# Performance work log

Measured on AMD Instinct MI355X. Metric: run time of the kernel, lower is better.

Reference implementation:

```python
import jax, jax.numpy as jnp
import numpy as np

B, S, D, H = 512, 128, 2, 512


def _lstm_cell(x, h, c, Wih, Whh, bih, bhh):
    # PyTorch gate order: i, f, g, o
    z = x @ Wih.T + h @ Whh.T + bih + bhh
    i, f, g, o = jnp.split(z, 4, axis=-1)
    c = jax.nn.sigmoid(f) * c + jax.nn.sigmoid(i) * jnp.tanh(g)
    h = jax.nn.sigmoid(o) * jnp.tanh(c)
    return h, c


def setup_inputs() -> dict:
    key = jax.random.key(0)
    ks = jax.random.split(key, 18)
    sc = 1.0 / np.sqrt(H)
    u = lambda k, shape: jax.random.uniform(k, shape, jnp.float32, -sc, sc)
    return {
        "inp": jax.random.normal(ks[0], (B, S, D), jnp.float32),
        "enc_Wih": u(ks[1], (4 * H, D)),
        "enc_Whh": u(ks[2], (4 * H, H)),
        "enc_bih": u(ks[3], (4 * H,)),
        "enc_bhh": u(ks[4], (4 * H,)),
        "dec_Wih": u(ks[5], (4 * H, D)),
        "dec_Whh": u(ks[6], (4 * H, H)),
        "dec_bih": u(ks[7], (4 * H,)),
        "dec_bhh": u(ks[8], (4 * H,)),
        "W1": u(ks[9], (H, H)),
        "b1": u(ks[10], (H,)),
        "W2": u(ks[11], (H, H)),
        "b2": u(ks[12], (H,)),
        "v_w": u(ks[13], (H,)),
        "v_b": u(ks[14], (1,)),
        "comb_W": u(ks[15], (H, 2 * H)),
        "comb_b": u(ks[16], (H,)),
    }


def reference(inp, enc_Wih, enc_Whh, enc_bih, enc_bhh,
              dec_Wih, dec_Whh, dec_bih, dec_bhh,
              W1, b1, W2, b2, v_w, v_b, comb_W, comb_b):
    Bb, Ss, _ = inp.shape
    xs = jnp.transpose(inp, (1, 0, 2))  # [S,B,D]

    # --- encoder LSTM (1 layer) ---
    def enc_step(carry, x):
        h, c = carry
        h, c = _lstm_cell(x, h, c, enc_Wih, enc_Whh, enc_bih, enc_bhh)
        return (h, c), h

    h0 = jnp.zeros((Bb, H), inp.dtype)
    (h_enc, c_enc), enc_out = jax.lax.scan(enc_step, (h0, h0), xs)  # enc_out: [S,B,H]

    W1e = enc_out @ W1.T + b1            # [S,B,H]
    enc_bt = jnp.transpose(enc_out, (1, 0, 2))  # [B,S,H]

    # --- pointer decoder ---
    def dec_step(carry, _):
        h, c, cur = carry
        h, c = _lstm_cell(cur, h, c, dec_Wih, dec_Whh, dec_bih, dec_bhh)
        q = h @ W2.T + b2                               # [B,H]
        u = jnp.tanh(W1e + q[None]) @ v_w + v_b[0]      # [S,B]
        a = jax.nn.softmax(u.T, axis=1)                 # [B,S]
        chosen = jnp.argmax(a, axis=1)                  # [B]
        cur = jnp.take_along_axis(inp, chosen[:, None, None], axis=1)[:, 0, :]  # [B,D]
        ctx = jnp.einsum('bs,bsh->bh', a, enc_bt)       # [B,H]
        h = jnp.concatenate([ctx, h], axis=1) @ comb_W.T + comb_b
        return (h, c, cur), a

    cur0 = jnp.full((Bb, D), -1.0, inp.dtype)
    _, outs = jax.lax.scan(dec_step, (h_enc, c_enc, cur0), None, length=Ss)
    return jnp.transpose(outs, (1, 0, 2))  # [B,S,S]
```

## Files before the change

### kernel.cpp

```cpp
#include <hip/hip_runtime.h>

#define PB 512
#define PS 128
#define PD 2
#define PH 512
#define P4H 2048

typedef unsigned int u32;
typedef unsigned short u16;
typedef __attribute__((ext_vector_type(8))) short short8;
typedef __attribute__((ext_vector_type(4))) float f32x4;

__device__ __forceinline__ float fast_sigmoid(float x) {
    return __fdividef(1.0f, 1.0f + __expf(-x));
}
__device__ __forceinline__ float fast_tanh(float x) {
    float ax = fabsf(x);
    float e = __expf(-2.0f * ax);
    float r = __fdividef(1.0f - e, 1.0f + e);
    return x < 0.0f ? -r : r;
}

__device__ __forceinline__ float bf_dec_u(u16 v) { return __uint_as_float((u32)v << 16); }
__device__ __forceinline__ u16 bf_trunc(float v) { return (u16)(__float_as_uint(v) >> 16); }
__device__ __forceinline__ u16 bf_rne(float v) {
    u32 u = __float_as_uint(v);
    return (u16)((u + 0x7FFFu + ((u >> 16) & 1u)) >> 16);
}
__device__ __forceinline__ void bf_split(float v, u16& hi, u16& lo) {
    hi = bf_trunc(v);
    lo = bf_rne(v - bf_dec_u(hi));
}

struct CF32 {
    using T = float;
    static __device__ __forceinline__ float dec(T v) { return v; }
    static __device__ __forceinline__ T enc(float v) { return v; }
    static __device__ __forceinline__ void dec4(const T* p, float* o) {
        float4 v = *(const float4*)p; o[0]=v.x; o[1]=v.y; o[2]=v.z; o[3]=v.w;
    }
};
struct CBF16 {
    using T = u16;
    static __device__ __forceinline__ float dec(T v) { return __uint_as_float((u32)v << 16); }
    static __device__ __forceinline__ T enc(float v) { return bf_rne(v); }
    static __device__ __forceinline__ void dec4(const T* p, float* o) {
        uint2 v = *(const uint2*)p;
        o[0] = __uint_as_float(v.x << 16);
        o[1] = __uint_as_float(v.x & 0xFFFF0000u);
        o[2] = __uint_as_float(v.y << 16);
        o[3] = __uint_as_float(v.y & 0xFFFF0000u);
    }
};

__global__ __launch_bounds__(256) void prep_whh(
    const float* __restrict__ Whh, u16* __restrict__ hi, u16* __restrict__ lo,
    float* __restrict__ f32out)
{
    int np = blockIdx.x;
    int j = np >> 2, g = np & 3;
    const float* src = Whh + (size_t)(g * PH + j) * PH;
    for (int k = threadIdx.x; k < PH; k += 256) {
        float v = src[k];
        u16 h_, l_;
        bf_split(v, h_, l_);
        hi[(size_t)np * PH + k] = h_;
        lo[(size_t)np * PH + k] = l_;
        if (f32out) f32out[(size_t)np * PH + k] = v;
    }
}
__global__ __launch_bounds__(256) void prep_split(
    const float* __restrict__ W, u16* __restrict__ hi, u16* __restrict__ lo, int K)
{
    int n = blockIdx.x;
    const float* src = W + (size_t)n * K;
    for (int k = threadIdx.x; k < K; k += 256) {
        u16 h_, l_;
        bf_split(src[k], h_, l_);
        hi[(size_t)n * K + k] = h_;
        lo[(size_t)n * K + k] = l_;
    }
}
__global__ __launch_bounds__(256) void prep_transpose_split(
    const float* __restrict__ W, u16* __restrict__ hi, u16* __restrict__ lo)
{
    __shared__ float tile[32][33];
    int m0 = blockIdx.x * 32;
    int k0 = blockIdx.y * 32;
    int tx = threadIdx.x & 31, ty = threadIdx.x >> 5;
    #pragma unroll
    for (int i = 0; i < 4; ++i) {
        int k = k0 + ty + i * 8;
        tile[ty + i * 8][tx] = W[(size_t)k * (2 * PH) + m0 + tx];
    }
    __syncthreads();
    #pragma unroll
    for (int i = 0; i < 4; ++i) {
        int m = m0 + ty + i * 8;
        float v = tile[tx][ty + i * 8];
        u16 h_, l_; bf_split(v, h_, l_);
        hi[(size_t)m * PH + k0 + tx] = h_;
        lo[(size_t)m * PH + k0 + tx] = l_;
    }
}
__global__ __launch_bounds__(256) void prep_small(
    const float* __restrict__ Wih, const float* __restrict__ bih,
    const float* __restrict__ bhh, float* __restrict__ wihp, float* __restrict__ bs)
{
    int np = blockIdx.x * 256 + threadIdx.x;
    if (np >= P4H) return;
    int j = np >> 2, g = np & 3;
    int n = g * PH + j;
    wihp[np * 2]     = Wih[(size_t)n * PD];
    wihp[np * 2 + 1] = Wih[(size_t)n * PD + 1];
    bs[np] = bih[n] + bhh[n];
}
__global__ __launch_bounds__(256) void prep_bfused(
    const float* __restrict__ whh_f32p, const float* __restrict__ comb_b,
    const float* __restrict__ bsum_d, float* __restrict__ bf)
{
    int np = blockIdx.x * 4 + (threadIdx.x >> 6);
    int lane = threadIdx.x & 63;
    const float* wr = whh_f32p + (size_t)np * PH + lane * 8;
    const float* cb = comb_b + lane * 8;
    float s = 0.0f;
    #pragma unroll
    for (int i = 0; i < 8; ++i) s += wr[i] * cb[i];
    #pragma unroll
    for (int off = 32; off; off >>= 1) s += __shfl_xor(s, off);
    if (lane == 0) bf[np] = s + bsum_d[np];
}

template<int EXTRA_MODE, int KK>
__global__ __launch_bounds__(256) void lstm_fused(
    const u16* __restrict__ Whh_hi, const u16* __restrict__ Whh_lo,
    const float* __restrict__ wih_perm, const float* __restrict__ bsum,
    const float* __restrict__ x, int x_stride,
    const float* __restrict__ h_in,
    float* __restrict__ cT,
    float* __restrict__ h_out,
    void* __restrict__ extra, int ex_stride)
{
    __shared__ u16 As_hi[64][72];
    __shared__ u16 As_lo[64][72];
    __shared__ u16 Bs_hi[64][72];
    __shared__ u16 Bs_lo[64][72];

    const int tid = threadIdx.x;
    const int bb = blockIdx.x * 64;
    const int bn = blockIdx.y * 64;
    const int w = tid >> 6;
    const int wm = w >> 1, wn = w & 1;
    const int lane = tid & 63;
    const int l15 = lane & 15, lq = lane >> 4;

    f32x4 acc[2][2];
    #pragma unroll
    for (int i = 0; i < 2; ++i)
        #pragma unroll
        for (int j = 0; j < 2; ++j)
            acc[i][j] = (f32x4)0.0f;

    for (int k0 = 0; k0 < KK; k0 += 64) {
        #pragma unroll
        for (int rep = 0; rep < 2; ++rep) {
            int chunk = tid + rep * 256;
            int row = chunk >> 3, kc = (chunk & 7) * 8;
            *(uint4*)&As_hi[row][kc] = *(const uint4*)&Whh_hi[(size_t)(bn + row) * KK + k0 + kc];
            *(uint4*)&As_lo[row][kc] = *(const uint4*)&Whh_lo[(size_t)(bn + row) * KK + k0 + kc];
        }
        #pragma unroll
        for (int rep = 0; rep < 4; ++rep) {
            int chunk = tid + rep * 256;
            int row = chunk >> 4, kc = (chunk & 15) * 4;
            float4 v = *(const float4*)&h_in[(size_t)(bb + row) * KK + k0 + kc];
            u16 h0_, l0_, h1_, l1_, h2_, l2_, h3_, l3_;
            bf_split(v.x, h0_, l0_); bf_split(v.y, h1_, l1_);
            bf_split(v.z, h2_, l2_); bf_split(v.w, h3_, l3_);
            *(uint2*)&Bs_hi[row][kc] = make_uint2((u32)h0_ | ((u32)h1_ << 16),
                                                  (u32)h2_ | ((u32)h3_ << 16));
            *(uint2*)&Bs_lo[row][kc] = make_uint2((u32)l0_ | ((u32)l1_ << 16),
                                                  (u32)l2_ | ((u32)l3_ << 16));
        }
        __syncthreads();
        #pragma unroll
        for (int ks = 0; ks < 2; ++ks) {
            int kk = ks * 32 + lq * 8;
            short8 ah[2], al[2], bh[2], bl[2];
            #pragma unroll
            for (int mf = 0; mf < 2; ++mf) {
                int r = wm * 32 + mf * 16 + l15;
                ah[mf] = *(const short8*)&As_hi[r][kk];
                al[mf] = *(const short8*)&As_lo[r][kk];
            }
            #pragma unroll
            for (int nf = 0; nf < 2; ++nf) {
                int r = wn * 32 + nf * 16 + l15;
                bh[nf] = *(const short8*)&Bs_hi[r][kk];
                bl[nf] = *(const short8*)&Bs_lo[r][kk];
            }
            #pragma unroll
            for (int mf = 0; mf < 2; ++mf)
                #pragma unroll
                for (int nf = 0; nf < 2; ++nf) {
                    acc[mf][nf] = __builtin_amdgcn_mfma_f32_16x16x32_bf16(ah[mf], bh[nf], acc[mf][nf], 0, 0, 0);
                    acc[mf][nf] = __builtin_amdgcn_mfma_f32_16x16x32_bf16(ah[mf], bl[nf], acc[mf][nf], 0, 0, 0);
                    acc[mf][nf] = __builtin_amdgcn_mfma_f32_16x16x32_bf16(al[mf], bh[nf], acc[mf][nf], 0, 0, 0);
                }
        }
        __syncthreads();
    }

    float* Hs = (float*)&As_hi[0][0];
    #pragma unroll
    for (int nf = 0; nf < 2; ++nf) {
        int b_loc = wn * 32 + nf * 16 + l15;
        int b = bb + b_loc;
        float x0 = x[b * x_stride];
        float x1 = x[b * x_stride + 1];
        #pragma unroll
        for (int mf = 0; mf < 2; ++mf) {
            int np_loc = wm * 32 + mf * 16 + lq * 4;
            int np = bn + np_loc;
            float4 b4 = *(const float4*)&bsum[np];
            float4 wA = *(const float4*)&wih_perm[np * 2];
            float4 wB = *(const float4*)&wih_perm[np * 2 + 4];
            float zi = acc[mf][nf][0] + b4.x + x0 * wA.x + x1 * wA.y;
            float zf = acc[mf][nf][1] + b4.y + x0 * wA.z + x1 * wA.w;
            float zg = acc[mf][nf][2] + b4.z + x0 * wB.x + x1 * wB.y;
            float zo = acc[mf][nf][3] + b4.w + x0 * wB.z + x1 * wB.w;
            int jg = np >> 2;
            float cold = cT[(size_t)jg * PB + b];
            float cv = fast_sigmoid(zf) * cold + fast_sigmoid(zi) * fast_tanh(zg);
            float hv = fast_sigmoid(zo) * fast_tanh(cv);
            cT[(size_t)jg * PB + b] = cv;
            Hs[(np_loc >> 2) * 66 + b_loc] = hv;
        }
    }
    __syncthreads();
    {
        int b_loc = tid >> 2, jp = (tid & 3) * 4;
        int b = bb + b_loc;
        int jbase = bn >> 2;
        float4 hv4;
        hv4.x = Hs[(jp + 0) * 66 + b_loc];
        hv4.y = Hs[(jp + 1) * 66 + b_loc];
        hv4.z = Hs[(jp + 2) * 66 + b_loc];
        hv4.w = Hs[(jp + 3) * 66 + b_loc];
        *(float4*)&h_out[(size_t)b * PH + jbase + jp] = hv4;
        if (EXTRA_MODE == 1) {
            u16* e = (u16*)extra;
            *(uint2*)&e[(size_t)b * ex_stride + jbase + jp] =
                make_uint2((u32)bf_rne(hv4.x) | ((u32)bf_rne(hv4.y) << 16),
                           (u32)bf_rne(hv4.z) | ((u32)bf_rne(hv4.w) << 16));
        } else if (EXTRA_MODE == 2) {
            float* e = (float*)extra;
            *(float4*)&e[(size_t)b * ex_stride + jbase + jp] = hv4;
        }
    }
}

template<int ACT_F32, int OUTMODE>
__global__ __launch_bounds__(256) void gemm_wtA(
    const u16* __restrict__ Whi, const u16* __restrict__ Wlo,
    const void* __restrict__ act, const float* __restrict__ bias,
    void* __restrict__ out, void* __restrict__ out2, int K, int ldo)
{
    __shared__ u16 As_hi[64][72];
    __shared__ u16 As_lo[64][72];
    __shared__ u16 Bs_hi[64][72];
    __shared__ u16 Bs_lo[64][72];

    const int tid = threadIdx.x;
    const int bm = blockIdx.x * 64;
    const int bn = blockIdx.y * 64;
    const int w = tid >> 6;
    const int wm = w >> 1, wn = w & 1;
    const int lane = tid & 63;
    const int l15 = lane & 15, lq = lane >> 4;

    f32x4 acc[2][2];
    #pragma unroll
    for (int i = 0; i < 2; ++i)
        #pragma unroll
        for (int j = 0; j < 2; ++j)
            acc[i][j] = (f32x4)0.0f;

    for (int k0 = 0; k0 < K; k0 += 64) {
        #pragma unroll
        for (int rep = 0; rep < 2; ++rep) {
            int chunk = tid + rep * 256;
            int row = chunk >> 3, kc = (chunk & 7) * 8;
            *(uint4*)&As_hi[row][kc] = *(const uint4*)&Whi[(size_t)(bn + row) * K + k0 + kc];
            *(uint4*)&As_lo[row][kc] = *(const uint4*)&Wlo[(size_t)(bn + row) * K + k0 + kc];
        }
        if (ACT_F32) {
            const float* a = (const float*)act;
            #pragma unroll
            for (int rep = 0; rep < 4; ++rep) {
                int chunk = tid + rep * 256;
                int row = chunk >> 4, kc = (chunk & 15) * 4;
                float4 v = *(const float4*)&a[(size_t)(bm + row) * K + k0 + kc];
                u16 h0_, l0_, h1_, l1_, h2_, l2_, h3_, l3_;
                bf_split(v.x, h0_, l0_); bf_split(v.y, h1_, l1_);
                bf_split(v.z, h2_, l2_); bf_split(v.w, h3_, l3_);
                *(uint2*)&Bs_hi[row][kc] = make_uint2((u32)h0_ | ((u32)h1_ << 16),
                                                      (u32)h2_ | ((u32)h3_ << 16));
                *(uint2*)&Bs_lo[row][kc] = make_uint2((u32)l0_ | ((u32)l1_ << 16),
                                                      (u32)l2_ | ((u32)l3_ << 16));
            }
        } else {
            const u16* a = (const u16*)act;
            #pragma unroll
            for (int rep = 0; rep < 2; ++rep) {
                int chunk = tid + rep * 256;
                int row = chunk >> 3, kc = (chunk & 7) * 8;
                *(uint4*)&Bs_hi[row][kc] = *(const uint4*)&a[(size_t)(bm + row) * K + k0 + kc];
            }
        }
        __syncthreads();
        #pragma unroll
        for (int ks = 0; ks < 2; ++ks) {
            int kk = ks * 32 + lq * 8;
            short8 ah[2], al[2], bh[2], bl[2];
            #pragma unroll
            for (int mf = 0; mf < 2; ++mf) {
                int r = wm * 32 + mf * 16 + l15;
                ah[mf] = *(const short8*)&As_hi[r][kk];
                al[mf] = *(const short8*)&As_lo[r][kk];
            }
            #pragma unroll
            for (int nf = 0; nf < 2; ++nf) {
                int r = wn * 32 + nf * 16 + l15;
                bh[nf] = *(const short8*)&Bs_hi[r][kk];
                if (ACT_F32) bl[nf] = *(const short8*)&Bs_lo[r][kk];
            }
            #pragma unroll
            for (int mf = 0; mf < 2; ++mf)
                #pragma unroll
                for (int nf = 0; nf < 2; ++nf) {
                    acc[mf][nf] = __builtin_amdgcn_mfma_f32_16x16x32_bf16(ah[mf], bh[nf], acc[mf][nf], 0, 0, 0);
                    if (ACT_F32) {
                        acc[mf][nf] = __builtin_amdgcn_mfma_f32_16x16x32_bf16(ah[mf], bl[nf], acc[mf][nf], 0, 0, 0);
                        acc[mf][nf] = __builtin_amdgcn_mfma_f32_16x16x32_bf16(al[mf], bh[nf], acc[mf][nf], 0, 0, 0);
                    } else {
                        acc[mf][nf] = __builtin_amdgcn_mfma_f32_16x16x32_bf16(al[mf], bh[nf], acc[mf][nf], 0, 0, 0);
                    }
                }
        }
        __syncthreads();
    }

    #pragma unroll
    for (int nf = 0; nf < 2; ++nf) {
        int m = bm + wn * 32 + nf * 16 + l15;
        #pragma unroll
        for (int mf = 0; mf < 2; ++mf) {
            int n = bn + wm * 32 + mf * 16 + lq * 4;
            float4 b4 = bias ? *(const float4*)&bias[n] : make_float4(0.f, 0.f, 0.f, 0.f);
            float v0 = acc[mf][nf][0] + b4.x;
            float v1 = acc[mf][nf][1] + b4.y;
            float v2 = acc[mf][nf][2] + b4.z;
            float v3 = acc[mf][nf][3] + b4.w;
            if (OUTMODE == 1) {
                u16* o = (u16*)out;
                *(uint2*)&o[(size_t)m * ldo + n] =
                    make_uint2((u32)bf_rne(v0) | ((u32)bf_rne(v1) << 16),
                               (u32)bf_rne(v2) | ((u32)bf_rne(v3) << 16));
            } else if (OUTMODE == 2) {
                u16 h0_, l0_, h1_, l1_, h2_, l2_, h3_, l3_;
                bf_split(v0, h0_, l0_); bf_split(v1, h1_, l1_);
                bf_split(v2, h2_, l2_); bf_split(v3, h3_, l3_);
                u16* oh = (u16*)out;
                u16* ol = (u16*)out2;
                *(uint2*)&oh[(size_t)m * ldo + n] =
                    make_uint2((u32)h0_ | ((u32)h1_ << 16), (u32)h2_ | ((u32)h3_ << 16));
                *(uint2*)&ol[(size_t)m * ldo + n] =
                    make_uint2((u32)l0_ | ((u32)l1_ << 16), (u32)l2_ | ((u32)l3_ << 16));
            } else {
                float* o = (float*)out;
                *(float4*)&o[(size_t)m * ldo + n] = make_float4(v0, v1, v2, v3);
            }
        }
    }
}

__global__ __launch_bounds__(256) void attn_fused(
    const u16* __restrict__ W1e,
    const u16* __restrict__ enc_out,
    const float* __restrict__ qv,
    const float* __restrict__ v_w, const float* __restrict__ v_b,
    const float* __restrict__ inp,
    float* __restrict__ out,
    float* __restrict__ cat_out,
    float* __restrict__ cur, int t)
{
    __shared__ float u_s[PS];
    __shared__ float a_s[PS];
    const int b = blockIdx.x;
    const int tid = threadIdx.x;
    const int w = tid >> 6, lane = tid & 63;

    float q8[8], v8[8];
    {
        const float* qr = qv + (size_t)b * PH + lane * 8;
        CF32::dec4(qr, q8); CF32::dec4(qr + 4, q8 + 4);
        const float* vr = v_w + lane * 8;
        CF32::dec4(vr, v8); CF32::dec4(vr + 4, v8 + 4);
    }
    const float vb = v_b[0];
    const u16* wbase = W1e + (size_t)b * PS * PH + lane * 8;
    #pragma unroll 2
    for (int i = 0; i < 32; ++i) {
        int s = w * 32 + i;
        const u16* row = wbase + (size_t)s * PH;
        float w8[8];
        CBF16::dec4(row, w8); CBF16::dec4(row + 4, w8 + 4);
        float sum = 0.0f;
        #pragma unroll
        for (int j = 0; j < 8; ++j) sum += v8[j] * fast_tanh(w8[j] + q8[j]);
        #pragma unroll
        for (int off = 32; off; off >>= 1) sum += __shfl_xor(sum, off);
        if (lane == 0) u_s[s] = sum + vb;
    }
    __syncthreads();
    if (w == 0) {
        float2 uv = make_float2(u_s[lane * 2], u_s[lane * 2 + 1]);
        float m = fmaxf(uv.x, uv.y);
        int mi = (uv.y > uv.x) ? (lane * 2 + 1) : (lane * 2);
        #pragma unroll
        for (int off = 32; off; off >>= 1) {
            float om = __shfl_xor(m, off);
            int oi = __shfl_xor(mi, off);
            if (om > m || (om == m && oi < mi)) { m = om; mi = oi; }
        }
        float e0 = __expf(uv.x - m);
        float e1 = __expf(uv.y - m);
        float ssum = e0 + e1;
        #pragma unroll
        for (int off = 32; off; off >>= 1) ssum += __shfl_xor(ssum, off);
        float inv = __fdividef(1.0f, ssum);
        float2 av = make_float2(e0 * inv, e1 * inv);
        a_s[lane * 2] = av.x; a_s[lane * 2 + 1] = av.y;
        *(float2*)&out[(size_t)b * PS * PS + (size_t)t * PS + lane * 2] = av;
        if (lane == 0) {
            cur[b * 2]     = inp[(size_t)b * PS * PD + mi * PD];
            cur[b * 2 + 1] = inp[(size_t)b * PS * PD + mi * PD + 1];
        }
    }
    __syncthreads();
    float acc0 = 0.0f, acc1 = 0.0f;
    const u16* ebase = enc_out + (size_t)b * PS * PH + tid * 2;
    #pragma unroll 4
    for (int s = 0; s < PS; ++s) {
        float a = a_s[s];
        u32 pr = *(const u32*)(ebase + (size_t)s * PH);
        acc0 = fmaf(a, __uint_as_float(pr << 16), acc0);
        acc1 = fmaf(a, __uint_as_float(pr & 0xFFFF0000u), acc1);
    }
    *(float2*)&cat_out[(size_t)b * (2 * PH) + tid * 2] = make_float2(acc0, acc1);
}

template<class C>
__global__ __launch_bounds__(256) void u_pass(
    const typename C::T* __restrict__ W1e, const float* __restrict__ q,
    const float* __restrict__ v_w, const float* __restrict__ v_b,
    float* __restrict__ u_t)
{
    int row = blockIdx.x * 4 + (threadIdx.x >> 6);
    int lane = threadIdx.x & 63;
    int s = row >> 9;
    int b = row & (PB - 1);
    const typename C::T* wr = W1e + (size_t)row * PH + lane * 8;
    const float* qr = q + (size_t)b * PH + lane * 8;
    const float* vr = v_w + lane * 8;
    float w8[8], q8[8], v8[8];
    C::dec4(wr, w8); C::dec4(wr + 4, w8 + 4);
    CF32::dec4(qr, q8); CF32::dec4(qr + 4, q8 + 4);
    CF32::dec4(vr, v8); CF32::dec4(vr + 4, v8 + 4);
    float sum = 0.0f;
    #pragma unroll
    for (int i = 0; i < 8; ++i)
        sum += v8[i] * fast_tanh(w8[i] + q8[i]);
    #pragma unroll
    for (int off = 32; off; off >>= 1) sum += __shfl_xor(sum, off);
    if (lane == 0) u_t[b * PS + s] = sum + v_b[0];
}

__global__ __launch_bounds__(256) void softmax_step(
    const float* __restrict__ u_t, const float* __restrict__ inp,
    float* __restrict__ a_buf, float* __restrict__ out,
    float* __restrict__ cur, int t)
{
    int b = blockIdx.x * 4 + (threadIdx.x >> 6);
    int lane = threadIdx.x & 63;
    float2 uv = *(const float2*)&u_t[b * PS + lane * 2];
    float m = fmaxf(uv.x, uv.y);
    int mi = (uv.y > uv.x) ? (lane * 2 + 1) : (lane * 2);
    #pragma unroll
    for (int off = 32; off; off >>= 1) {
        float om = __shfl_xor(m, off);
        int oi = __shfl_xor(mi, off);
        if (om > m || (om == m && oi < mi)) { m = om; mi = oi; }
    }
    float e0 = __expf(uv.x - m);
    float e1 = __expf(uv.y - m);
    float ssum = e0 + e1;
    #pragma unroll
    for (int off = 32; off; off >>= 1) ssum += __shfl_xor(ssum, off);
    float inv = __fdividef(1.0f, ssum);
    float2 av = make_float2(e0 * inv, e1 * inv);
    *(float2*)&a_buf[b * PS + lane * 2] = av;
    *(float2*)&out[(size_t)b * PS * PS + (size_t)t * PS + lane * 2] = av;
    if (lane == 0) {
        cur[b * 2]     = inp[(size_t)b * PS * PD + mi * PD];
        cur[b * 2 + 1] = inp[(size_t)b * PS * PD + mi * PD + 1];
    }
}

template<class C>
__global__ __launch_bounds__(256) void ctx_kernel(
    const typename C::T* __restrict__ enc_out, const float* __restrict__ a_buf,
    float* __restrict__ catbuf)
{
    int b = blockIdx.x;
    int hidx = threadIdx.x;
    const float* ab = a_buf + b * PS;
    const typename C::T* e = enc_out + (size_t)b * PH;
    float acc0 = 0.0f, acc1 = 0.0f;
    #pragma unroll 4
    for (int s = 0; s < PS; ++s) {
        float a = ab[s];
        const typename C::T* es = e + (size_t)s * PB * PH;
        acc0 = fmaf(a, C::dec(es[hidx]), acc0);
        acc1 = fmaf(a, C::dec(es[hidx + 256]), acc1);
    }
    catbuf[(size_t)b * (2 * PH) + hidx] = acc0;
    catbuf[(size_t)b * (2 * PH) + hidx + 256] = acc1;
}

__global__ __launch_bounds__(256) void init_kernel(
    float* __restrict__ h, float* __restrict__ c, float* __restrict__ cur)
{
    int i = blockIdx.x * 256 + threadIdx.x;
    if (i < PB * PH) { h[i] = 0.0f; c[i] = 0.0f; }
    if (i < PB * PD) cur[i] = -1.0f;
}

template<class CA, class CO, int BM, int BN, int BK, int TM, int TN>
__global__ __launch_bounds__(256) void gemm_nt(
    const typename CA::T* __restrict__ A, const float* __restrict__ Bm,
    const float* __restrict__ bias, typename CO::T* __restrict__ C,
    int M, int N, int K)
{
    __shared__ float As[BK][BM];
    __shared__ float Bs[BK][BN];
    constexpr int TCOLS = BN / TN;
    constexpr int TROWS = BM / TM;
    static_assert(TCOLS * TROWS == 256, "thread tiling");
    const int tid = threadIdx.x;
    const int tc = tid % TCOLS;
    const int tr = tid / TCOLS;
    const int bm = blockIdx.y * BM;
    const int bn = blockIdx.x * BN;
    constexpr int AF4 = BM * BK / 4;
    constexpr int BF4 = BN * BK / 4;
    constexpr int KQ  = BK / 4;
    float acc[TM][TN];
    #pragma unroll
    for (int m = 0; m < TM; ++m)
        #pragma unroll
        for (int n = 0; n < TN; ++n) acc[m][n] = 0.0f;
    for (int k0 = 0; k0 < K; k0 += BK) {
        #pragma unroll
        for (int i = tid; i < AF4; i += 256) {
            int r = i / KQ, kq = i % KQ;
            float v4[4];
            CA::dec4(A + (size_t)(bm + r) * K + k0 + kq * 4, v4);
            As[kq*4+0][r] = v4[0]; As[kq*4+1][r] = v4[1];
            As[kq*4+2][r] = v4[2]; As[kq*4+3][r] = v4[3];
        }
        #pragma unroll
        for (int i = tid; i < BF4; i += 256) {
            int r = i / KQ, kq = i % KQ;
            const float4 v = *(const float4*)(Bm + (size_t)(bn + r) * K + k0 + kq * 4);
            Bs[kq*4+0][r] = v.x; Bs[kq*4+1][r] = v.y;
            Bs[kq*4+2][r] = v.z; Bs[kq*4+3][r] = v.w;
        }
        __syncthreads();
        #pragma unroll
        for (int k = 0; k < BK; ++k) {
            float av[TM], bv[TN];
            #pragma unroll
            for (int m = 0; m < TM; ++m) av[m] = As[k][tr * TM + m];
            #pragma unroll
            for (int n = 0; n < TN; ++n) bv[n] = Bs[k][tc * TN + n];
            #pragma unroll
            for (int m = 0; m < TM; ++m)
                #pragma unroll
                for (int n = 0; n < TN; ++n)
                    acc[m][n] = fmaf(av[m], bv[n], acc[m][n]);
        }
        __syncthreads();
    }
    #pragma unroll
    for (int m = 0; m < TM; ++m) {
        int row = bm + tr * TM + m;
        #pragma unroll
        for (int n = 0; n < TN; ++n) {
            int col = bn + tc * TN + n;
            float v = acc[m][n];
            if (bias) v += bias[col];
            C[(size_t)row * N + col] = CO::enc(v);
        }
    }
}

template<class CE>
__global__ __launch_bounds__(256) void lstm_cell(
    const float* __restrict__ z,
    const float* __restrict__ x, int x_stride,
    const float* __restrict__ Wih,
    const float* __restrict__ bih, const float* __restrict__ bhh,
    float* __restrict__ c, float* __restrict__ h,
    typename CE::T* __restrict__ extra, int extra_stride)
{
    int idx = blockIdx.x * 256 + threadIdx.x;
    int b = idx >> 9, j = idx & (PH - 1);
    float x0 = x[b * x_stride];
    float x1 = x[b * x_stride + 1];
    const float* zr = z + (size_t)b * P4H;
    float zi = zr[j]        + bih[j]        + bhh[j]        + x0 * Wih[2*j]          + x1 * Wih[2*j+1];
    float zf = zr[j + PH]   + bih[j + PH]   + bhh[j + PH]   + x0 * Wih[2*(j+PH)]     + x1 * Wih[2*(j+PH)+1];
    float zg = zr[j + 2*PH] + bih[j + 2*PH] + bhh[j + 2*PH] + x0 * Wih[2*(j+2*PH)]   + x1 * Wih[2*(j+2*PH)+1];
    float zo = zr[j + 3*PH] + bih[j + 3*PH] + bhh[j + 3*PH] + x0 * Wih[2*(j+3*PH)]   + x1 * Wih[2*(j+3*PH)+1];
    float cv = fast_sigmoid(zf) * c[idx] + fast_sigmoid(zi) * fast_tanh(zg);
    float hv = fast_sigmoid(zo) * fast_tanh(cv);
    c[idx] = cv;
    h[idx] = hv;
    if (extra) extra[(size_t)b * extra_stride + j] = CE::enc(hv);
}

struct Inputs {
    const float *inp, *enc_Wih, *enc_Whh, *enc_bih, *enc_bhh;
    const float *dec_Wih, *dec_Whh, *dec_bih, *dec_bhh;
    const float *W1, *b1, *W2, *b2, *v_w, *v_b, *comb_W, *comb_b;
};
static Inputs unpack(void* const* d_in) {
    Inputs in;
    in.inp = (const float*)d_in[0];
    in.enc_Wih = (const float*)d_in[1]; in.enc_Whh = (const float*)d_in[2];
    in.enc_bih = (const float*)d_in[3]; in.enc_bhh = (const float*)d_in[4];
    in.dec_Wih = (const float*)d_in[5]; in.dec_Whh = (const float*)d_in[6];
    in.dec_bih = (const float*)d_in[7]; in.dec_bhh = (const float*)d_in[8];
    in.W1 = (const float*)d_in[9];  in.b1 = (const float*)d_in[10];
    in.W2 = (const float*)d_in[11]; in.b2 = (const float*)d_in[12];
    in.v_w = (const float*)d_in[13]; in.v_b = (const float*)d_in[14];
    in.comb_W = (const float*)d_in[15]; in.comb_b = (const float*)d_in[16];
    return in;
}

static const size_t BIG = (size_t)PS * PB * PH;

static void run_mfma2(const Inputs& in, float* out, void* d_ws, hipStream_t stream)
{
    char* p = (char*)d_ws;
    auto alloc = [&](size_t bytes) { char* r = p; p += bytes; return r; };
    u16* enc_out  = (u16*)alloc(BIG * 2);
    u16* W1e      = (u16*)alloc(BIG * 2);
    u16* whh_e_hi = (u16*)alloc((size_t)P4H * PH * 2);
    u16* whh_e_lo = (u16*)alloc((size_t)P4H * PH * 2);
    u16* whh_d_hi = (u16*)alloc((size_t)P4H * PH * 2);
    u16* whh_d_lo = (u16*)alloc((size_t)P4H * PH * 2);
    u16* w1h = (u16*)alloc((size_t)PH * PH * 2);
    u16* w1l = (u16*)alloc((size_t)PH * PH * 2);
    u16* w2h = (u16*)alloc((size_t)PH * PH * 2);
    u16* w2l = (u16*)alloc((size_t)PH * PH * 2);
    u16* ctw_h = (u16*)alloc((size_t)(2 * PH) * PH * 2);
    u16* ctw_l = (u16*)alloc((size_t)(2 * PH) * PH * 2);
    u16* wf_h = (u16*)alloc((size_t)P4H * (2 * PH) * 2);
    u16* wf_l = (u16*)alloc((size_t)P4H * (2 * PH) * 2);
    float* wih_e = (float*)alloc((size_t)P4H * 2 * 4);
    float* wih_d = (float*)alloc((size_t)P4H * 2 * 4);
    float* bsum_e = (float*)alloc((size_t)P4H * 4);
    float* bsum_d = (float*)alloc((size_t)P4H * 4);
    float* b_fus  = (float*)alloc((size_t)P4H * 4);
    float* hpp0 = (float*)alloc((size_t)PB * PH * 4);
    float* hpp1 = (float*)alloc((size_t)PB * PH * 4);
    float* cT   = (float*)alloc((size_t)PB * PH * 4);
    float* catreg = (float*)alloc((size_t)PB * 2 * PH * 4 * 2);
    float* cur  = (float*)alloc((size_t)PB * PD * 4);
    float* whh_f32p = catreg;
    float* h0 = (float*)whh_e_hi;
    float* q  = (float*)whh_e_lo;
    float* cat[2] = { catreg, catreg + (size_t)PB * 2 * PH };
    float* hpp[2] = { hpp0, hpp1 };

    prep_whh<<<P4H, 256, 0, stream>>>(in.enc_Whh, whh_e_hi, whh_e_lo, nullptr);
    prep_whh<<<P4H, 256, 0, stream>>>(in.dec_Whh, whh_d_hi, whh_d_lo, whh_f32p);
    prep_split<<<PH, 256, 0, stream>>>(in.W1, w1h, w1l, PH);
    prep_split<<<PH, 256, 0, stream>>>(in.W2, w2h, w2l, PH);
    prep_transpose_split<<<dim3(32, 16), 256, 0, stream>>>(in.comb_W, ctw_h, ctw_l);
    prep_small<<<P4H / 256, 256, 0, stream>>>(in.enc_Wih, in.enc_bih, in.enc_bhh, wih_e, bsum_e);
    prep_small<<<P4H / 256, 256, 0, stream>>>(in.dec_Wih, in.dec_bih, in.dec_bhh, wih_d, bsum_d);
    gemm_wtA<1, 2><<<dim3(P4H / 64, (2 * PH) / 64), 256, 0, stream>>>(
        ctw_h, ctw_l, whh_f32p, nullptr, wf_h, wf_l, PH, 2 * PH);
    prep_bfused<<<P4H / 4, 256, 0, stream>>>(whh_f32p, in.comb_b, bsum_d, b_fus);
    init_kernel<<<1024, 256, 0, stream>>>(hpp0, cT, cur);

    for (int s = 0; s < PS; ++s) {
        lstm_fused<1, PH><<<dim3(PB / 64, P4H / 64), 256, 0, stream>>>(
            whh_e_hi, whh_e_lo, wih_e, bsum_e,
            in.inp + s * PD, PS * PD,
            hpp[s & 1], cT, hpp[(s + 1) & 1],
            enc_out + (size_t)s * PH, PS * PH);
    }

    gemm_wtA<0, 1><<<dim3((PS * PB) / 64, PH / 64), 256, 0, stream>>>(
        w1h, w1l, enc_out, in.b1, W1e, nullptr, PH, PH);

    for (int t = 0; t < PS; ++t) {
        float* cat_out = cat[(t + 1) & 1];
        if (t == 0) {
            lstm_fused<2, PH><<<dim3(PB / 64, P4H / 64), 256, 0, stream>>>(
                whh_d_hi, whh_d_lo, wih_d, bsum_d,
                cur, PD, hpp[0], cT, h0, cat_out + PH, 2 * PH);
        } else {
            lstm_fused<2, 2 * PH><<<dim3(PB / 64, P4H / 64), 256, 0, stream>>>(
                wf_h, wf_l, wih_d, b_fus,
                cur, PD, cat[t & 1], cT, h0, cat_out + PH, 2 * PH);
        }
        gemm_wtA<1, 0><<<dim3(PB / 64, PH / 64), 256, 0, stream>>>(
            w2h, w2l, h0, in.b2, q, nullptr, PH, PH);
        attn_fused<<<PB, 256, 0, stream>>>(
            W1e, enc_out, q, in.v_w, in.v_b, in.inp, out, cat_out, cur, t);
    }
}

static void run_mfma(const Inputs& in, float* out, void* d_ws, hipStream_t stream)
{
    char* p = (char*)d_ws;
    auto alloc = [&](size_t bytes) { char* r = p; p += bytes; return r; };
    u16* enc_out = (u16*)alloc(BIG * 2);
    u16* W1e     = (u16*)alloc(BIG * 2);
    u16* whh_e_hi = (u16*)alloc((size_t)P4H * PH * 2);
    u16* whh_e_lo = (u16*)alloc((size_t)P4H * PH * 2);
    u16* whh_d_hi = (u16*)alloc((size_t)P4H * PH * 2);
    u16* whh_d_lo = (u16*)alloc((size_t)P4H * PH * 2);
    u16* w1h = (u16*)alloc((size_t)PH * PH * 2);
    u16* w1l = (u16*)alloc((size_t)PH * PH * 2);
    u16* w2h = (u16*)alloc((size_t)PH * PH * 2);
    u16* w2l = (u16*)alloc((size_t)PH * PH * 2);
    u16* cwh = (u16*)alloc((size_t)PH * 2 * PH * 2);
    u16* cwl = (u16*)alloc((size_t)PH * 2 * PH * 2);
    float* wih_e = (float*)alloc((size_t)P4H * 2 * 4);
    float* wih_d = (float*)alloc((size_t)P4H * 2 * 4);
    float* bsum_e = (float*)alloc((size_t)P4H * 4);
    float* bsum_d = (float*)alloc((size_t)P4H * 4);
    float* hpp0 = (float*)alloc((size_t)PB * PH * 4);
    float* hpp1 = (float*)alloc((size_t)PB * PH * 4);
    float* cT   = (float*)alloc((size_t)PB * PH * 4);
    float* h0   = (float*)alloc((size_t)PB * PH * 4);
    float* q    = (float*)alloc((size_t)PB * PH * 4);
    float* catbuf = (float*)alloc((size_t)PB * 2 * PH * 4);
    float* u_t  = (float*)alloc((size_t)PB * PS * 4);
    float* a_buf = (float*)alloc((size_t)PB * PS * 4);
    float* cur  = (float*)alloc((size_t)PB * PD * 4);
    float* hpp[2] = { hpp0, hpp1 };

    prep_whh<<<P4H, 256, 0, stream>>>(in.enc_Whh, whh_e_hi, whh_e_lo, nullptr);
    prep_whh<<<P4H, 256, 0, stream>>>(in.dec_Whh, whh_d_hi, whh_d_lo, nullptr);
    prep_split<<<PH, 256, 0, stream>>>(in.W1, w1h, w1l, PH);
    prep_split<<<PH, 256, 0, stream>>>(in.W2, w2h, w2l, PH);
    prep_split<<<PH, 256, 0, stream>>>(in.comb_W, cwh, cwl, 2 * PH);
    prep_small<<<P4H / 256, 256, 0, stream>>>(in.enc_Wih, in.enc_bih, in.enc_bhh, wih_e, bsum_e);
    prep_small<<<P4H / 256, 256, 0, stream>>>(in.dec_Wih, in.dec_bih, in.dec_bhh, wih_d, bsum_d);
    init_kernel<<<1024, 256, 0, stream>>>(hpp0, cT, cur);

    for (int s = 0; s < PS; ++s) {
        lstm_fused<1, PH><<<dim3(PB / 64, P4H / 64), 256, 0, stream>>>(
            whh_e_hi, whh_e_lo, wih_e, bsum_e,
            in.inp + s * PD, PS * PD,
            hpp[s & 1], cT, hpp[(s + 1) & 1],
            enc_out + (size_t)s * PB * PH, PH);
    }
    gemm_wtA<0, 1><<<dim3((PS * PB) / 64, PH / 64), 256, 0, stream>>>(
        w1h, w1l, enc_out, in.b1, W1e, nullptr, PH, PH);
    for (int t = 0; t < PS; ++t) {
        lstm_fused<2, PH><<<dim3(PB / 64, P4H / 64), 256, 0, stream>>>(
            whh_d_hi, whh_d_lo, wih_d, bsum_d,
            cur, PD, hpp[t & 1], cT, h0, catbuf + PH, 2 * PH);
        gemm_wtA<1, 0><<<dim3(PB / 64, PH / 64), 256, 0, stream>>>(
            w2h, w2l, h0, in.b2, q, nullptr, PH, PH);
        u_pass<CBF16><<<(PS * PB) / 4, 256, 0, stream>>>(W1e, q, in.v_w, in.v_b, u_t);
        softmax_step<<<PB / 4, 256, 0, stream>>>(u_t, in.inp, a_buf, out, cur, t);
        ctx_kernel<CBF16><<<PB, 256, 0, stream>>>(enc_out, a_buf, catbuf);
        gemm_wtA<1, 0><<<dim3(PB / 64, PH / 64), 256, 0, stream>>>(
            cwh, cwl, catbuf, in.comb_b, hpp[(t + 1) & 1], nullptr, 2 * PH, PH);
    }
}

static void run_fallback(const Inputs& in, float* out, void* d_ws, hipStream_t stream)
{
    char* p = (char*)d_ws;
    u16* enc_out = (u16*)p;  p += BIG * 2;
    u16* W1e     = (u16*)p;  p += BIG * 2;
    float* ws = (float*)p;
    size_t off = 0;
    auto alloc = [&](size_t n) { float* r = ws + off; off += n; return r; };
    float* z      = alloc((size_t)PB * P4H);
    float* h      = alloc((size_t)PB * PH);
    float* c      = alloc((size_t)PB * PH);
    float* h0     = alloc((size_t)PB * PH);
    float* q      = alloc((size_t)PB * PH);
    float* catbuf = alloc((size_t)PB * 2 * PH);
    float* u_t    = alloc((size_t)PB * PS);
    float* a_buf  = alloc((size_t)PB * PS);
    float* cur    = alloc((size_t)PB * PD);

    init_kernel<<<1024, 256, 0, stream>>>(h, c, cur);
    for (int s = 0; s < PS; ++s) {
        gemm_nt<CF32, CF32, 64, 64, 32, 4, 4><<<dim3(P4H / 64, PB / 64), 256, 0, stream>>>(
            h, in.enc_Whh, nullptr, z, PB, P4H, PH);
        lstm_cell<CBF16><<<1024, 256, 0, stream>>>(
            z, in.inp + s * PD, PS * PD, in.enc_Wih, in.enc_bih, in.enc_bhh,
            c, h, enc_out + (size_t)s * PB * PH, PH);
    }
    gemm_nt<CBF16, CBF16, 64, 64, 32, 4, 4><<<dim3(PH / 64, (PS * PB) / 64), 256, 0, stream>>>(
        enc_out, in.W1, in.b1, W1e, PS * PB, PH, PH);
    for (int t = 0; t < PS; ++t) {
        gemm_nt<CF32, CF32, 64, 64, 32, 4, 4><<<dim3(P4H / 64, PB / 64), 256, 0, stream>>>(
            h, in.dec_Whh, nullptr, z, PB, P4H, PH);
        lstm_cell<CF32><<<1024, 256, 0, stream>>>(
            z, cur, PD, in.dec_Wih, in.dec_bih, in.dec_bhh,
            c, h0, catbuf + PH, 2 * PH);
        gemm_nt<CF32, CF32, 32, 32, 32, 2, 2><<<dim3(PH / 32, PB / 32), 256, 0, stream>>>(
            h0, in.W2, in.b2, q, PB, PH, PH);
        u_pass<CBF16><<<(PS * PB) / 4, 256, 0, stream>>>(W1e, q, in.v_w, in.v_b, u_t);
        softmax_step<<<PB / 4, 256, 0, stream>>>(u_t, in.inp, a_buf, out, cur, t);
        ctx_kernel<CBF16><<<PB, 256, 0, stream>>>(enc_out, a_buf, catbuf);
        gemm_nt<CF32, CF32, 32, 32, 32, 2, 2><<<dim3(PH / 32, PB / 32), 256, 0, stream>>>(
            catbuf, in.comb_W, in.comb_b, h, PB, PH, 2 * PH);
    }
}

extern "C" void kernel_launch(void* const* d_in, const int* in_sizes, int n_in,
                              void* d_out, int out_size, void* d_ws, size_t ws_size,
                              hipStream_t stream)
{
    Inputs in = unpack(d_in);
    float* out = (float*)d_out;

    const size_t t1_need =
        BIG * 2 * 2 +
        (size_t)P4H * PH * 2 * 4 +
        (size_t)PH * PH * 2 * 4 +
        (size_t)(2 * PH) * PH * 2 * 2 +
        (size_t)P4H * (2 * PH) * 2 * 2 +
        (size_t)P4H * 2 * 4 * 2 +
        (size_t)P4H * 4 * 3 +
        (size_t)PB * PH * 4 * 3 +
        (size_t)PB * 2 * PH * 4 * 2 +
        (size_t)PB * PD * 4;
    const size_t t2_need =
        BIG * 2 * 2 +
        (size_t)P4H * PH * 2 * 4 +
        (size_t)PH * PH * 2 * 4 +
        (size_t)PH * 2 * PH * 2 * 2 +
        (size_t)P4H * 2 * 4 * 2 +
        (size_t)P4H * 4 * 2 +
        ((size_t)PB * PH * 6 + (size_t)PB * PS * 2 + PB * PD) * 4;
    const size_t t3_need =
        BIG * 2 * 2 +
        ((size_t)PB * P4H + 4 * (size_t)PB * PH + (size_t)PB * 2 * PH +
         2 * (size_t)PB * PS + (size_t)PB * PD) * 4;

    if (ws_size >= t1_need)       run_mfma2(in, out, d_ws, stream);
    else if (ws_size >= t2_need)  run_mfma(in, out, d_ws, stream);
    else if (ws_size >= t3_need)  run_fallback(in, out, d_ws, stream);
}
```

Baseline: 11.78 ms.

## Use 32-row LSTM and q GEMM tiles to raise block count

Adds lstm_fused32, which tiles 32 gate rows by 64 batch rows, and gemm32_f32, which uses 32x32 tiles. Both replace the 64x64 kernels in the encoder and decoder loops, doubling or quadrupling the number of blocks per launch so more CUs are busy on these small per-step GEMMs. Workspace is reorganized: the encoder Whh split, the transposed comb_W and one h ping-pong buffer are aliased into the W1e region, which is only written after the encoder finishes. The cost is smaller tiles with less operand reuse per block, and the aliasing depends on W1e not being produced before the encoder loop ends.

```diff
diff --git a/kernel.cpp b/kernel.cpp
--- a/kernel.cpp
+++ b/kernel.cpp
@@ -129,6 +129,180 @@
     #pragma unroll
     for (int off = 32; off; off >>= 1) s += __shfl_xor(s, off);
     if (lane == 0) bf[np] = s + bsum_d[np];
+}
+
+template<int EXTRA_MODE, int KK>
+__global__ __launch_bounds__(256, 2) void lstm_fused32(
+    const u16* __restrict__ Whh_hi, const u16* __restrict__ Whh_lo,
+    const float* __restrict__ wih_perm, const float* __restrict__ bsum,
+    const float* __restrict__ x, int x_stride,
+    const float* __restrict__ h_in,
+    float* __restrict__ cT,
+    float* __restrict__ h_out,
+    void* __restrict__ extra, int ex_stride)
+{
+    __shared__ u16 As_hi[32][72];
+    __shared__ u16 As_lo[32][72];
+    __shared__ u16 Bs_hi[64][72];
+    __shared__ u16 Bs_lo[64][72];
+
+    const int tid = threadIdx.x;
+    const int bnp = blockIdx.x * 32;
+    const int bb  = blockIdx.y * 64;
+    const int w = tid >> 6;
+    const int wm = w >> 1, wn = w & 1;
+    const int lane = tid & 63;
+    const int l15 = lane & 15, lq = lane >> 4;
+
+    f32x4 acc0 = (f32x4)0.0f, acc1 = (f32x4)0.0f;
+
+    for (int k0 = 0; k0 < KK; k0 += 64) {
+        {
+            int row = tid >> 3, kc = (tid & 7) * 8;
+            *(uint4*)&As_hi[row][kc] = *(const uint4*)&Whh_hi[(size_t)(bnp + row) * KK + k0 + kc];
+            *(uint4*)&As_lo[row][kc] = *(const uint4*)&Whh_lo[(size_t)(bnp + row) * KK + k0 + kc];
+        }
+        #pragma unroll
+        for (int rep = 0; rep < 4; ++rep) {
+            int chunk = tid + rep * 256;
+            int row = chunk >> 4, kc = (chunk & 15) * 4;
+            float4 v = *(const float4*)&h_in[(size_t)(bb + row) * KK + k0 + kc];
+            u16 h0_, l0_, h1_, l1_, h2_, l2_, h3_, l3_;
+            bf_split(v.x, h0_, l0_); bf_split(v.y, h1_, l1_);
+            bf_split(v.z, h2_, l2_); bf_split(v.w, h3_, l3_);
+            *(uint2*)&Bs_hi[row][kc] = make_uint2((u32)h0_ | ((u32)h1_ << 16),
+                                                  (u32)h2_ | ((u32)h3_ << 16));
+            *(uint2*)&Bs_lo[row][kc] = make_uint2((u32)l0_ | ((u32)l1_ << 16),
+                                                  (u32)l2_ | ((u32)l3_ << 16));
+        }
+        __syncthreads();
+        #pragma unroll
+        for (int ks = 0; ks < 2; ++ks) {
+            int kk = ks * 32 + lq * 8;
+            short8 ah, al, bh0, bl0, bh1, bl1;
+            {
+                int r = wm * 16 + l15;
+                ah = *(const short8*)&As_hi[r][kk];
+                al = *(const short8*)&As_lo[r][kk];
+            }
+            {
+                int r = wn * 32 + l15;
+                bh0 = *(const short8*)&Bs_hi[r][kk];
+                bl0 = *(const short8*)&Bs_lo[r][kk];
+                bh1 = *(const short8*)&Bs_hi[r + 16][kk];
+                bl1 = *(const short8*)&Bs_lo[r + 16][kk];
+            }
+            acc0 = __builtin_amdgcn_mfma_f32_16x16x32_bf16(ah, bh0, acc0, 0, 0, 0);
+            acc0 = __builtin_amdgcn_mfma_f32_16x16x32_bf16(ah, bl0, acc0, 0, 0, 0);
+            acc0 = __builtin_amdgcn_mfma_f32_16x16x32_bf16(al, bh0, acc0, 0, 0, 0);
+            acc1 = __builtin_amdgcn_mfma_f32_16x16x32_bf16(ah, bh1, acc1, 0, 0, 0);
+            acc1 = __builtin_amdgcn_mfma_f32_16x16x32_bf16(ah, bl1, acc1, 0, 0, 0);
+            acc1 = __builtin_amdgcn_mfma_f32_16x16x32_bf16(al, bh1, acc1, 0, 0, 0);
+        }
+        __syncthreads();
+    }
+
+    float* Hs = (float*)&As_hi[0][0];
+    const int np_loc = wm * 16 + lq * 4;
+    const int np = bnp + np_loc;
+    const float4 b4 = *(const float4*)&bsum[np];
+    const float4 wA = *(const float4*)&wih_perm[np * 2];
+    const float4 wB = *(const float4*)&wih_perm[np * 2 + 4];
+    const int jg = np >> 2;
+    #pragma unroll
+    for (int nf = 0; nf < 2; ++nf) {
+        int b_loc = wn * 32 + nf * 16 + l15;
+        int b = bb + b_loc;
+        float x0 = x[b * x_stride];
+        float x1 = x[b * x_stride + 1];
+        f32x4 a = nf ? acc1 : acc0;
+        float zi = a[0] + b4.x + x0 * wA.x + x1 * wA.y;
+        float zf = a[1] + b4.y + x0 * wA.z + x1 * wA.w;
+        float zg = a[2] + b4.z + x0 * wB.x + x1 * wB.y;
+        float zo = a[3] + b4.w + x0 * wB.z + x1 * wB.w;
+        float cold = cT[(size_t)jg * PB + b];
+        float cv = fast_sigmoid(zf) * cold + fast_sigmoid(zi) * fast_tanh(zg);
+        float hv = fast_sigmoid(zo) * fast_tanh(cv);
+        cT[(size_t)jg * PB + b] = cv;
+        Hs[(np_loc >> 2) * 66 + b_loc] = hv;
+    }
+    __syncthreads();
+    {
+        int b_loc = tid & 63, jp = (tid >> 6) * 2;
+        int b = bb + b_loc;
+        int jbase = bnp >> 2;
+        float h0v = Hs[jp * 66 + b_loc];
+        float h1v = Hs[(jp + 1) * 66 + b_loc];
+        *(float2*)&h_out[(size_t)b * PH + jbase + jp] = make_float2(h0v, h1v);
+        if (EXTRA_MODE == 1) {
+            u16* e = (u16*)extra;
+            *(u32*)&e[(size_t)b * ex_stride + jbase + jp] =
+                (u32)bf_rne(h0v) | ((u32)bf_rne(h1v) << 16);
+        } else if (EXTRA_MODE == 2) {
+            float* e = (float*)extra;
+            *(float2*)&e[(size_t)b * ex_stride + jbase + jp] = make_float2(h0v, h1v);
+        }
+    }
+}
+
+__global__ __launch_bounds__(256, 2) void gemm32_f32(
+    const u16* __restrict__ Whi, const u16* __restrict__ Wlo,
+    const float* __restrict__ act, const float* __restrict__ bias,
+    float* __restrict__ out, int K, int ldo)
+{
+    __shared__ u16 As_hi[32][72];
+    __shared__ u16 As_lo[32][72];
+    __shared__ u16 Bs_hi[32][72];
+    __shared__ u16 Bs_lo[32][72];
+
+    const int tid = threadIdx.x;
+    const int bn = blockIdx.x * 32;
+    const int bm = blockIdx.y * 32;
+    const int w = tid >> 6;
+    const int wm = w >> 1, wn = w & 1;
+    const int lane = tid & 63, l15 = lane & 15, lq = lane >> 4;
+
+    f32x4 acc = (f32x4)0.0f;
+
+    for (int k0 = 0; k0 < K; k0 += 64) {
+        {
+            int row = tid >> 3, kc = (tid & 7) * 8;
+            *(uint4*)&As_hi[row][kc] = *(const uint4*)&Whi[(size_t)(bn + row) * K + k0 + kc];
+            *(uint4*)&As_lo[row][kc] = *(const uint4*)&Wlo[(size_t)(bn + row) * K + k0 + kc];
+        }
+        #pragma unroll
+        for (int rep = 0; rep < 2; ++rep) {
+            int chunk = tid + rep * 256;
+            int row = chunk >> 4, kc = (chunk & 15) * 4;
+            float4 v = *(const float4*)&act[(size_t)(bm + row) * K + k0 + kc];
+            u16 h0_, l0_, h1_, l1_, h2_, l2_, h3_, l3_;
+            bf_split(v.x, h0_, l0_); bf_split(v.y, h1_, l1_);
+            bf_split(v.z, h2_, l2_); bf_split(v.w, h3_, l3_);
+            *(uint2*)&Bs_hi[row][kc] = make_uint2((u32)h0_ | ((u32)h1_ << 16),
+                                                  (u32)h2_ | ((u32)h3_ << 16));
+            *(uint2*)&Bs_lo[row][kc] = make_uint2((u32)l0_ | ((u32)l1_ << 16),
+                                                  (u32)l2_ | ((u32)l3_ << 16));
+        }
+        __syncthreads();
+        #pragma unroll
+        for (int ks = 0; ks < 2; ++ks) {
+            int kk = ks * 32 + lq * 8;
+            short8 ah = *(const short8*)&As_hi[wm * 16 + l15][kk];
+            short8 al = *(const short8*)&As_lo[wm * 16 + l15][kk];
+            short8 bh = *(const short8*)&Bs_hi[wn * 16 + l15][kk];
+            short8 bl = *(const short8*)&Bs_lo[wn * 16 + l15][kk];
+            acc = __builtin_amdgcn_mfma_f32_16x16x32_bf16(ah, bh, acc, 0, 0, 0);
+            acc = __builtin_amdgcn_mfma_f32_16x16x32_bf16(ah, bl, acc, 0, 0, 0);
+            acc = __builtin_amdgcn_mfma_f32_16x16x32_bf16(al, bh, acc, 0, 0, 0);
+        }
+        __syncthreads();
+    }
+
+    int m = bm + wn * 16 + l15;
+    int n = bn + wm * 16 + lq * 4;
+    float4 b4 = bias ? *(const float4*)&bias[n] : make_float4(0.f, 0.f, 0.f, 0.f);
+    *(float4*)&out[(size_t)m * ldo + n] =
+        make_float4(acc[0] + b4.x, acc[1] + b4.y, acc[2] + b4.z, acc[3] + b4.w);
 }
 
 template<int EXTRA_MODE, int KK>
@@ -667,17 +841,14 @@
     char* p = (char*)d_ws;
     auto alloc = [&](size_t bytes) { char* r = p; p += bytes; return r; };
     u16* enc_out  = (u16*)alloc(BIG * 2);
-    u16* W1e      = (u16*)alloc(BIG * 2);
-    u16* whh_e_hi = (u16*)alloc((size_t)P4H * PH * 2);
-    u16* whh_e_lo = (u16*)alloc((size_t)P4H * PH * 2);
+    char* W1e_reg = alloc(BIG * 2);
+    u16* W1e = (u16*)W1e_reg;
     u16* whh_d_hi = (u16*)alloc((size_t)P4H * PH * 2);
     u16* whh_d_lo = (u16*)alloc((size_t)P4H * PH * 2);
     u16* w1h = (u16*)alloc((size_t)PH * PH * 2);
     u16* w1l = (u16*)alloc((size_t)PH * PH * 2);
     u16* w2h = (u16*)alloc((size_t)PH * PH * 2);
     u16* w2l = (u16*)alloc((size_t)PH * PH * 2);
-    u16* ctw_h = (u16*)alloc((size_t)(2 * PH) * PH * 2);
-    u16* ctw_l = (u16*)alloc((size_t)(2 * PH) * PH * 2);
     u16* wf_h = (u16*)alloc((size_t)P4H * (2 * PH) * 2);
     u16* wf_l = (u16*)alloc((size_t)P4H * (2 * PH) * 2);
     float* wih_e = (float*)alloc((size_t)P4H * 2 * 4);
@@ -686,13 +857,20 @@
     float* bsum_d = (float*)alloc((size_t)P4H * 4);
     float* b_fus  = (float*)alloc((size_t)P4H * 4);
     float* hpp0 = (float*)alloc((size_t)PB * PH * 4);
-    float* hpp1 = (float*)alloc((size_t)PB * PH * 4);
     float* cT   = (float*)alloc((size_t)PB * PH * 4);
+    float* h0   = (float*)alloc((size_t)PB * PH * 4);
+    float* q    = (float*)alloc((size_t)PB * PH * 4);
     float* catreg = (float*)alloc((size_t)PB * 2 * PH * 4 * 2);
     float* cur  = (float*)alloc((size_t)PB * PD * 4);
+
+    u16* ctw_h = (u16*)W1e_reg;
+    u16* ctw_l = (u16*)(W1e_reg + 2097152);
+    u16* whh_e_hi = (u16*)(W1e_reg + 2 * 2097152);
+    u16* whh_e_lo = (u16*)(W1e_reg + 2 * 2097152 + 2097152);
+    whh_e_hi = (u16*)(W1e_reg + 4194304);
+    whh_e_lo = (u16*)(W1e_reg + 4194304 + 2097152);
+    float* hpp1 = (float*)(W1e_reg + 4194304 + 2 * 2097152);
     float* whh_f32p = catreg;
-    float* h0 = (float*)whh_e_hi;
-    float* q  = (float*)whh_e_lo;
     float* cat[2] = { catreg, catreg + (size_t)PB * 2 * PH };
     float* hpp[2] = { hpp0, hpp1 };
 
@@ -709,7 +887,7 @@
     init_kernel<<<1024, 256, 0, stream>>>(hpp0, cT, cur);
 
     for (int s = 0; s < PS; ++s) {
-        lstm_fused<1, PH><<<dim3(PB / 64, P4H / 64), 256, 0, stream>>>(
+        lstm_fused32<1, PH><<<dim3(P4H / 32, PB / 64), 256, 0, stream>>>(
             whh_e_hi, whh_e_lo, wih_e, bsum_e,
             in.inp + s * PD, PS * PD,
             hpp[s & 1], cT, hpp[(s + 1) & 1],
@@ -722,16 +900,16 @@
     for (int t = 0; t < PS; ++t) {
         float* cat_out = cat[(t + 1) & 1];
         if (t == 0) {
-            lstm_fused<2, PH><<<dim3(PB / 64, P4H / 64), 256, 0, stream>>>(
+            lstm_fused32<2, PH><<<dim3(P4H / 32, PB / 64), 256, 0, stream>>>(
                 whh_d_hi, whh_d_lo, wih_d, bsum_d,
                 cur, PD, hpp[0], cT, h0, cat_out + PH, 2 * PH);
         } else {
-            lstm_fused<2, 2 * PH><<<dim3(PB / 64, P4H / 64), 256, 0, stream>>>(
+            lstm_fused32<2, 2 * PH><<<dim3(P4H / 32, PB / 64), 256, 0, stream>>>(
                 wf_h, wf_l, wih_d, b_fus,
                 cur, PD, cat[t & 1], cT, h0, cat_out + PH, 2 * PH);
         }
-        gemm_wtA<1, 0><<<dim3(PB / 64, PH / 64), 256, 0, stream>>>(
-            w2h, w2l, h0, in.b2, q, nullptr, PH, PH);
+        gemm32_f32<<<dim3(PH / 32, PB / 32), 256, 0, stream>>>(
+            w2h, w2l, h0, in.b2, q, PH, PH);
         attn_fused<<<PB, 256, 0, stream>>>(
             W1e, enc_out, q, in.v_w, in.v_b, in.inp, out, cat_out, cur, t);
     }
@@ -853,13 +1031,12 @@
 
     const size_t t1_need =
         BIG * 2 * 2 +
-        (size_t)P4H * PH * 2 * 4 +
+        (size_t)P4H * PH * 2 * 2 +
         (size_t)PH * PH * 2 * 4 +
-        (size_t)(2 * PH) * PH * 2 * 2 +
         (size_t)P4H * (2 * PH) * 2 * 2 +
         (size_t)P4H * 2 * 4 * 2 +
         (size_t)P4H * 4 * 3 +
-        (size_t)PB * PH * 4 * 3 +
+        (size_t)PB * PH * 4 * 4 +
         (size_t)PB * 2 * PH * 4 * 2 +
         (size_t)PB * PD * 4;
     const size_t t2_need =
```

Measured after the change: 10.79 ms. 1.09x faster.
